# Kernel tuning notes

Hardware: AMD Instinct MI355X
Metric: run time of the kernel (lower is better)

The kernel has to match this reference:

```python
import jax, jax.numpy as jnp
import numpy as np

H = 16       # num_heads
D = 128      # head_dim
SCALE = 1.0 / np.sqrt(D).astype(np.float32)


def setup_inputs() -> dict:
    key = jax.random.key(0)
    ks = jax.random.split(key, 5)
    B, S, C = 2, 2048, 2048
    x = jax.random.normal(ks[0], (B, S, C), dtype=jnp.float32)
    # nn.Linear stores weight as [out_features, in_features]; scale ~ kaiming-ish
    s = 1.0 / np.sqrt(C)
    wq = jax.random.normal(ks[1], (C, C), dtype=jnp.float32) * s
    wk = jax.random.normal(ks[2], (C, C), dtype=jnp.float32) * s
    wv = jax.random.normal(ks[3], (C, C), dtype=jnp.float32) * s
    wo = jax.random.normal(ks[4], (C, C), dtype=jnp.float32) * s
    return {"x": x, "wq": wq, "wk": wk, "wv": wv, "wo": wo}


def reference(x, wq, wk, wv, wo):
    B, S, C = x.shape
    # projections: nn.Linear(x) = x @ W.T
    q = (x @ wq.T).reshape(B, S, H, D).transpose(0, 2, 1, 3)  # [B,H,S,D]
    k = (x @ wk.T).reshape(B, S, H, D).transpose(0, 2, 1, 3)
    v = (x @ wv.T).reshape(B, S, H, D).transpose(0, 2, 1, 3)
    scores = jnp.einsum('bhqd,bhkd->bhqk', q, k) * SCALE      # [B,H,S,S]
    attn = jax.nn.softmax(scores, axis=-1)
    out = jnp.einsum('bhqk,bhkd->bhqd', attn, v)              # [B,H,S,D]
    out = out.transpose(0, 2, 1, 3).reshape(B, S, H * D)
    return out @ wo.T
```

## Files before the change

### kernel.cpp

```cpp
#include <hip/hip_runtime.h>
#include <hip/hip_bf16.h>
#include <cstdint>
#include <cstddef>

typedef __bf16 bf16_t;
typedef __bf16 bf8_t __attribute__((ext_vector_type(8)));
typedef __bf16 bf4_t __attribute__((ext_vector_type(4)));
typedef float f4_t __attribute__((ext_vector_type(4)));
typedef float f8_t __attribute__((ext_vector_type(8)));

#define DEV static __device__ __forceinline__

DEV f4_t mfma16(bf8_t a, bf8_t b, f4_t c) {
    return __builtin_amdgcn_mfma_f32_16x16x32_bf16(a, b, c, 0, 0, 0);
}

DEV bf8_t cvt8(f8_t v) {
    bf8_t r;
#pragma unroll
    for (int i = 0; i < 8; ++i) r[i] = (bf16_t)v[i];
    return r;
}

DEV void load_lds16(const bf16_t* g, bf16_t* l) {
    __builtin_amdgcn_global_load_lds(
        (const __attribute__((address_space(1))) uint32_t*)g,
        (__attribute__((address_space(3))) uint32_t*)l,
        16, 0, 0);
}

__global__ __launch_bounds__(256) void cvt_fused(const float* __restrict__ x,
                                                 const float* __restrict__ wq,
                                                 const float* __restrict__ wk,
                                                 const float* __restrict__ wv,
                                                 bf16_t* __restrict__ xb,
                                                 bf16_t* __restrict__ wqkvb) {
    const int bid = blockIdx.x;
    const float* src;
    bf16_t* dst;
    int base;
    if (bid < 4096) {
        src = x; dst = xb; base = bid;
    } else {
        const int seg = (bid - 4096) >> 11;
        src = (seg == 0) ? wq : (seg == 1) ? wk : wv;
        dst = wqkvb + (size_t)seg * 4194304;
        base = (bid - 4096) & 2047;
    }
    const size_t i = ((size_t)base * 256 + threadIdx.x) * 8;
    const f8_t v = *(const f8_t*)&src[i];
    *(bf8_t*)&dst[i] = cvt8(v);
}

__global__ __launch_bounds__(256) void cvt_bf16(const float* __restrict__ in,
                                                bf16_t* __restrict__ out, int n8) {
    const int i = blockIdx.x * 256 + threadIdx.x;
    if (i < n8) {
        const f8_t v = *(const f8_t*)&in[(size_t)i * 8];
        *(bf8_t*)&out[(size_t)i * 8] = cvt8(v);
    }
}

DEV void stage_half(const bf16_t* X, int row0, int rb, int kt, bf16_t* bufX,
                    int wave, int srow, int scol) {
#pragma unroll
    for (int kk = 0; kk < 2; ++kk)
        load_lds16(X + (size_t)(row0 + rb + wave * 16 + srow) * 2048 + kt * 64 + kk * 32 + scol,
                   bufX + kk * 8192 + (rb + wave * 16) * 32);
}

__global__ __launch_bounds__(512, 2) void gemm_qk(const bf16_t* __restrict__ A,
                                                  const bf16_t* __restrict__ B,
                                                  bf16_t* __restrict__ Cq,
                                                  bf16_t* __restrict__ Ck) {
    __shared__ bf16_t smem[65536];

    const int tid = threadIdx.x, lane = tid & 63, wave = tid >> 6;
    const int wr = wave >> 2, wc = wave & 3;
    const int q4 = lane >> 4, r16 = lane & 15;
    const int srow = lane >> 2;
    const int scol = ((lane & 3) ^ ((lane >> 3) & 3)) * 8;
    const int rkey = (r16 >> 1) & 3;

    int wg = blockIdx.y * 16 + blockIdx.x;
    wg = (wg & 7) * 32 + (wg >> 3);
    const int bm0 = (wg / 16) * 256;
    const int bn0 = (wg % 16) * 256;

    f4_t acc[8][4] = {};

    {
        bf16_t* b0 = smem;
        bf16_t* b1 = smem + 32768;
        stage_half(A, bm0, 0,   0, b0,          wave, srow, scol);
        stage_half(A, bm0, 128, 0, b0,          wave, srow, scol);
        stage_half(B, bn0, 0,   0, b0 + 16384,  wave, srow, scol);
        stage_half(B, bn0, 128, 0, b0 + 16384,  wave, srow, scol);
        stage_half(B, bn0, 0,   1, b1 + 16384,  wave, srow, scol);
        stage_half(B, bn0, 128, 1, b1 + 16384,  wave, srow, scol);
        asm volatile("s_waitcnt vmcnt(4)" ::: "memory");
        __builtin_amdgcn_s_barrier();
    }

    for (int t = 0; t < 32; ++t) {
        bf16_t* buf  = smem + (t & 1) * 32768;
        bf16_t* bufN = smem + ((t + 1) & 1) * 32768;

        bf8_t bq[4][2];
#pragma unroll
        for (int p = 0; p < 4; ++p) {
            if (p == 0) {
#pragma unroll
                for (int n = 0; n < 4; ++n)
#pragma unroll
                    for (int kk = 0; kk < 2; ++kk)
                        bq[n][kk] = *(const bf8_t*)&buf[16384 + kk * 8192 +
                                                       (wc * 64 + n * 16 + r16) * 32 +
                                                       (q4 ^ rkey) * 8];
            }
            bf8_t af[2][2];
#pragma unroll
            for (int i = 0; i < 2; ++i)
#pragma unroll
                for (int kk = 0; kk < 2; ++kk)
                    af[i][kk] = *(const bf8_t*)&buf[kk * 8192 +
                                                    (wr * 128 + (2 * p + i) * 16 + r16) * 32 +
                                                    (q4 ^ rkey) * 8];

            if (p == 0 && t + 1 < 32) {
                stage_half(A, bm0, 0,   t + 1, bufN, wave, srow, scol);
                stage_half(A, bm0, 128, t + 1, bufN, wave, srow, scol);
            }
            if (p == 1 && t + 2 < 32)
                stage_half(B, bn0, 0,   t + 2, buf + 16384, wave, srow, scol);
            if (p == 2 && t + 2 < 32)
                stage_half(B, bn0, 128, t + 2, buf + 16384, wave, srow, scol);

            __builtin_amdgcn_s_barrier();
            asm volatile("s_waitcnt lgkmcnt(0)" ::: "memory");
            __builtin_amdgcn_s_setprio(1);
#pragma unroll
            for (int kk = 0; kk < 2; ++kk)
#pragma unroll
                for (int i = 0; i < 2; ++i)
#pragma unroll
                    for (int n = 0; n < 4; ++n)
                        acc[2 * p + i][n] = mfma16(af[i][kk], bq[n][kk], acc[2 * p + i][n]);
            __builtin_amdgcn_s_setprio(0);
            if (p == 3) {
                if (t < 30) {
                    asm volatile("s_waitcnt vmcnt(4)" ::: "memory");
                } else {
                    asm volatile("s_waitcnt vmcnt(0)" ::: "memory");
                }
            }
            __builtin_amdgcn_s_barrier();
        }
    }

    __syncthreads();

    bf16_t* strip = smem + wave * 4608;
    bf16_t* dst = (bn0 < 2048) ? Cq : Ck;
    const int nb = (bn0 & 2047) + wc * 64;
#pragma unroll
    for (int P = 0; P < 2; ++P) {
#pragma unroll
        for (int i = 0; i < 4; ++i)
#pragma unroll
            for (int n = 0; n < 4; ++n)
#pragma unroll
                for (int r = 0; r < 4; ++r)
                    strip[(i * 16 + q4 * 4 + r) * 72 + n * 16 + r16] =
                        (bf16_t)acc[P * 4 + i][n][r];
        asm volatile("s_waitcnt lgkmcnt(0)" ::: "memory");
#pragma unroll
        for (int it = 0; it < 8; ++it) {
            const int row = it * 8 + (lane >> 3);
            const int c = (lane & 7) * 8;
            *(bf8_t*)&dst[(size_t)(bm0 + wr * 128 + P * 64 + row) * 2048 + nb + c] =
                *(const bf8_t*)&strip[row * 72 + c];
        }
        asm volatile("s_waitcnt lgkmcnt(0)" ::: "memory");
    }
}

__global__ __launch_bounds__(512, 2) void gemm_v(const bf16_t* __restrict__ A,
                                                 const bf16_t* __restrict__ B,
                                                 bf16_t* __restrict__ Cv) {
    __shared__ bf16_t smem[73728];

    const int tid = threadIdx.x, lane = tid & 63, wave = tid >> 6;
    const int wr = wave >> 2, wc = wave & 3;
    const int q4 = lane >> 4, r16 = lane & 15;
    const int srow = lane >> 2;
    const int scol = ((lane & 3) ^ ((lane >> 3) & 3)) * 8;
    const int rkey = (r16 >> 1) & 3;

    int wg = blockIdx.y * 8 + blockIdx.x;
    wg = (wg & 7) * 32 + (wg >> 3);
    const int bm0 = (wg / 8) * 128;
    const int bn0 = (wg % 8) * 256;

    f4_t acc[4][4] = {};

    auto stageA = [&](int kt, bf16_t* buf) {
#pragma unroll
        for (int kk = 0; kk < 2; ++kk)
            load_lds16(A + (size_t)(bm0 + wave * 16 + srow) * 2048 + kt * 64 + kk * 32 + scol,
                       buf + kk * 4096 + wave * 16 * 32);
    };
    auto stageB = [&](int kt, bf16_t* buf, int rb) {
#pragma unroll
        for (int kk = 0; kk < 2; ++kk)
            load_lds16(B + (size_t)(bn0 + rb + wave * 16 + srow) * 2048 + kt * 64 + kk * 32 + scol,
                       buf + 8192 + kk * 8192 + (rb + wave * 16) * 32);
    };

    {
        stageA(0, smem);
        stageB(0, smem, 0);
        stageB(0, smem, 128);
        stageA(1, smem + 24576);
        stageB(1, smem + 24576, 0);
        stageB(1, smem + 24576, 128);
        asm volatile("s_waitcnt vmcnt(6)" ::: "memory");
        __builtin_amdgcn_s_barrier();
    }

    int cb = 0, sb = 2;
    for (int t = 0; t < 32; ++t) {
        bf16_t* buf  = smem + cb * 24576;
        bf16_t* sbuf = smem + sb * 24576;

        {
            bf8_t af[4], bq[4];
#pragma unroll
            for (int i = 0; i < 4; ++i)
                af[i] = *(const bf8_t*)&buf[(wr * 64 + i * 16 + r16) * 32 + (q4 ^ rkey) * 8];
#pragma unroll
            for (int n = 0; n < 4; ++n)
                bq[n] = *(const bf8_t*)&buf[8192 + (wc * 64 + n * 16 + r16) * 32 +
                                            (q4 ^ rkey) * 8];
            if (t + 2 < 32) {
                stageA(t + 2, sbuf);
                stageB(t + 2, sbuf, 0);
            }
            __builtin_amdgcn_s_barrier();
            asm volatile("s_waitcnt lgkmcnt(0)" ::: "memory");
            __builtin_amdgcn_s_setprio(1);
#pragma unroll
            for (int i = 0; i < 4; ++i)
#pragma unroll
                for (int n = 0; n < 4; ++n)
                    acc[i][n] = mfma16(af[i], bq[n], acc[i][n]);
            __builtin_amdgcn_s_setprio(0);
            __builtin_amdgcn_s_barrier();
        }

        {
            bf8_t af[4], bq[4];
#pragma unroll
            for (int i = 0; i < 4; ++i)
                af[i] = *(const bf8_t*)&buf[4096 + (wr * 64 + i * 16 + r16) * 32 +
                                            (q4 ^ rkey) * 8];
#pragma unroll
            for (int n = 0; n < 4; ++n)
                bq[n] = *(const bf8_t*)&buf[8192 + 8192 + (wc * 64 + n * 16 + r16) * 32 +
                                            (q4 ^ rkey) * 8];
            if (t + 2 < 32)
                stageB(t + 2, sbuf, 128);
            __builtin_amdgcn_s_barrier();
            asm volatile("s_waitcnt lgkmcnt(0)" ::: "memory");
            __builtin_amdgcn_s_setprio(1);
#pragma unroll
            for (int i = 0; i < 4; ++i)
#pragma unroll
                for (int n = 0; n < 4; ++n)
                    acc[i][n] = mfma16(af[i], bq[n], acc[i][n]);
            __builtin_amdgcn_s_setprio(0);
            if (t < 30) {
                asm volatile("s_waitcnt vmcnt(6)" ::: "memory");
            } else {
                asm volatile("s_waitcnt vmcnt(0)" ::: "memory");
            }
            __builtin_amdgcn_s_barrier();
        }

        cb = (cb == 2) ? 0 : cb + 1;
        sb = (sb == 2) ? 0 : sb + 1;
    }

    __syncthreads();

    bf16_t* strip = smem + wave * 4608;
    const int bb = bm0 >> 11;
    const int s0 = (bm0 & 2047) + wr * 64;
#pragma unroll
    for (int i = 0; i < 4; ++i)
#pragma unroll
        for (int n = 0; n < 4; ++n)
#pragma unroll
            for (int r = 0; r < 4; ++r)
                strip[(n * 16 + r16) * 72 + i * 16 + q4 * 4 + r] =
                    (bf16_t)acc[i][n][r];
    asm volatile("s_waitcnt lgkmcnt(0)" ::: "memory");
#pragma unroll
    for (int it = 0; it < 8; ++it) {
        const int nrow = it * 8 + (lane >> 3);
        const int c = (lane & 7) * 8;
        const int dg = bn0 + wc * 64 + nrow;
        const int h = dg >> 7, d = dg & 127;
        *(bf8_t*)&Cv[(((size_t)(bb * 16 + h) * 128 + d) << 11) + s0 + c] =
            *(const bf8_t*)&strip[nrow * 72 + c];
    }
}

__global__ __launch_bounds__(512, 2) void gemm_out(const bf16_t* __restrict__ A,
                                                   const bf16_t* __restrict__ B,
                                                   float* __restrict__ C) {
    __shared__ bf16_t smem[73728];

    const int tid = threadIdx.x, lane = tid & 63, wave = tid >> 6;
    const int wr = wave >> 2, wc = wave & 3;
    const int q4 = lane >> 4, r16 = lane & 15;
    const int srow = lane >> 2;
    const int scol = ((lane & 3) ^ ((lane >> 3) & 3)) * 8;
    const int rkey = (r16 >> 1) & 3;

    int wg = blockIdx.y * 8 + blockIdx.x;
    wg = (wg & 7) * 32 + (wg >> 3);
    const int bm0 = (wg / 8) * 128;
    const int bn0 = (wg % 8) * 256;

    f4_t acc[4][4] = {};

    auto stageA = [&](int kt, bf16_t* buf) {
#pragma unroll
        for (int kk = 0; kk < 2; ++kk)
            load_lds16(A + (size_t)(bm0 + wave * 16 + srow) * 2048 + kt * 64 + kk * 32 + scol,
                       buf + kk * 4096 + wave * 16 * 32);
    };
    auto stageB = [&](int kt, bf16_t* buf, int rb) {
#pragma unroll
        for (int kk = 0; kk < 2; ++kk)
            load_lds16(B + (size_t)(bn0 + rb + wave * 16 + srow) * 2048 + kt * 64 + kk * 32 + scol,
                       buf + 8192 + kk * 8192 + (rb + wave * 16) * 32);
    };

    {
        stageA(0, smem);
        stageB(0, smem, 0);
        stageB(0, smem, 128);
        stageA(1, smem + 24576);
        stageB(1, smem + 24576, 0);
        stageB(1, smem + 24576, 128);
        asm volatile("s_waitcnt vmcnt(6)" ::: "memory");
        __builtin_amdgcn_s_barrier();
    }

    int cb = 0, sb = 2;
    for (int t = 0; t < 32; ++t) {
        bf16_t* buf  = smem + cb * 24576;
        bf16_t* sbuf = smem + sb * 24576;

        {
            bf8_t af[4], bq[4];
#pragma unroll
            for (int i = 0; i < 4; ++i)
                af[i] = *(const bf8_t*)&buf[(wr * 64 + i * 16 + r16) * 32 + (q4 ^ rkey) * 8];
#pragma unroll
            for (int n = 0; n < 4; ++n)
                bq[n] = *(const bf8_t*)&buf[8192 + (wc * 64 + n * 16 + r16) * 32 +
                                            (q4 ^ rkey) * 8];
            if (t + 2 < 32) {
                stageA(t + 2, sbuf);
                stageB(t + 2, sbuf, 0);
            }
            __builtin_amdgcn_s_barrier();
            asm volatile("s_waitcnt lgkmcnt(0)" ::: "memory");
            __builtin_amdgcn_s_setprio(1);
#pragma unroll
            for (int i = 0; i < 4; ++i)
#pragma unroll
                for (int n = 0; n < 4; ++n)
                    acc[i][n] = mfma16(af[i], bq[n], acc[i][n]);
            __builtin_amdgcn_s_setprio(0);
            __builtin_amdgcn_s_barrier();
        }

        {
            bf8_t af[4], bq[4];
#pragma unroll
            for (int i = 0; i < 4; ++i)
                af[i] = *(const bf8_t*)&buf[4096 + (wr * 64 + i * 16 + r16) * 32 +
                                            (q4 ^ rkey) * 8];
#pragma unroll
            for (int n = 0; n < 4; ++n)
                bq[n] = *(const bf8_t*)&buf[8192 + 8192 + (wc * 64 + n * 16 + r16) * 32 +
                                            (q4 ^ rkey) * 8];
            if (t + 2 < 32)
                stageB(t + 2, sbuf, 128);
            __builtin_amdgcn_s_barrier();
            asm volatile("s_waitcnt lgkmcnt(0)" ::: "memory");
            __builtin_amdgcn_s_setprio(1);
#pragma unroll
            for (int i = 0; i < 4; ++i)
#pragma unroll
                for (int n = 0; n < 4; ++n)
                    acc[i][n] = mfma16(af[i], bq[n], acc[i][n]);
            __builtin_amdgcn_s_setprio(0);
            if (t < 30) {
                asm volatile("s_waitcnt vmcnt(6)" ::: "memory");
            } else {
                asm volatile("s_waitcnt vmcnt(0)" ::: "memory");
            }
            __builtin_amdgcn_s_barrier();
        }

        cb = (cb == 2) ? 0 : cb + 1;
        sb = (sb == 2) ? 0 : sb + 1;
    }

#pragma unroll
    for (int i = 0; i < 4; ++i)
#pragma unroll
        for (int n = 0; n < 4; ++n)
#pragma unroll
            for (int r = 0; r < 4; ++r) {
                const int m = bm0 + wr * 64 + i * 16 + q4 * 4 + r;
                const int nn = bn0 + wc * 64 + n * 16 + r16;
                C[(size_t)m * 2048 + nn] = acc[i][n][r];
            }
}

__global__ __launch_bounds__(256) void flash5(const bf16_t* __restrict__ Q,
                                              const bf16_t* __restrict__ K,
                                              const bf16_t* __restrict__ VT,
                                              bf16_t* __restrict__ O) {
    constexpr int S = 2048, C = 2048;
    constexpr float SCL = 0.08838834764831845f * 1.4426950408889634f;
    __shared__ bf16_t Ks[4 * 64 * 32];
    __shared__ bf16_t Vs[2 * 128 * 32];
    __shared__ bf16_t Ps[4][32 * 72];

    const int tid = threadIdx.x, lane = tid & 63, wave = tid >> 6;
    const int q4 = lane >> 4, r16 = lane & 15;
    const int bh = blockIdx.y, b = bh >> 4, h = bh & 15;
    const int q0 = blockIdx.x * 128 + wave * 32;

    const size_t qrow = (size_t)b * S + q0;
    const bf16_t* Qp0 = Q + (qrow + r16) * C + h * 128;
    const bf16_t* Qp1 = Q + (qrow + 16 + r16) * C + h * 128;
    const bf16_t* Kbase = K + (size_t)b * S * C + h * 128;
    const bf16_t* Vbase = VT + (size_t)bh * 128 * S;
    bf16_t* Pw = &Ps[wave][0];

    const int srow = lane >> 2;
    const int scol = (((lane & 3) ^ ((lane >> 3) & 3))) * 8;
    const int rkey = (r16 >> 1) & 3;

    bf8_t aq0[4], aq1[4];
#pragma unroll
    for (int kk = 0; kk < 4; ++kk) {
        aq0[kk] = *(const bf8_t*)&Qp0[kk * 32 + q4 * 8];
        aq1[kk] = *(const bf8_t*)&Qp1[kk * 32 + q4 * 8];
    }

    bf8_t ones;
#pragma unroll
    for (int i = 0; i < 8; ++i) ones[i] = (bf16_t)1.0f;

    f4_t o0[8] = {}, o1[8] = {};
    f4_t lacc0 = {}, lacc1 = {};

    for (int kv0 = 0; kv0 < S; kv0 += 64) {
        __syncthreads();
#pragma unroll
        for (int r0 = 0; r0 < 64; r0 += 16)
            load_lds16(Kbase + (size_t)(kv0 + r0 + srow) * C + wave * 32 + scol,
                       Ks + wave * 2048 + r0 * 32);
        {
            const int kkp = wave >> 1;
            const int rb = (wave & 1) * 64;
#pragma unroll
            for (int r0 = 0; r0 < 64; r0 += 16)
                load_lds16(Vbase + (size_t)(rb + r0 + srow) * S + kv0 + kkp * 32 + scol,
                           Vs + kkp * 4096 + (rb + r0) * 32);
        }
        __syncthreads();

        f4_t s4a[4] = {}, s4b[4] = {};
#pragma unroll
        for (int kk = 0; kk < 4; ++kk) {
#pragma unroll
            for (int j = 0; j < 4; ++j) {
                const bf8_t bk =
                    *(const bf8_t*)&Ks[kk * 2048 + (j * 16 + r16) * 32 + (q4 ^ rkey) * 8];
                s4a[j] = mfma16(bk, aq0[kk], s4a[j]);
                s4b[j] = mfma16(bk, aq1[kk], s4b[j]);
            }
        }

#pragma unroll
        for (int j = 0; j < 4; ++j) {
            bf4_t pa, pb;
#pragma unroll
            for (int r = 0; r < 4; ++r) {
                pa[r] = (bf16_t)exp2f(s4a[j][r] * SCL);
                pb[r] = (bf16_t)exp2f(s4b[j][r] * SCL);
            }
            *(bf4_t*)&Pw[r16 * 72 + j * 16 + q4 * 4] = pa;
            *(bf4_t*)&Pw[(16 + r16) * 72 + j * 16 + q4 * 4] = pb;
        }
        asm volatile("s_waitcnt lgkmcnt(0)" ::: "memory");

        bf8_t ap0[2], ap1[2];
#pragma unroll
        for (int kkp = 0; kkp < 2; ++kkp) {
            ap0[kkp] = *(const bf8_t*)&Pw[r16 * 72 + kkp * 32 + q4 * 8];
            ap1[kkp] = *(const bf8_t*)&Pw[(16 + r16) * 72 + kkp * 32 + q4 * 8];
        }

#pragma unroll
        for (int kkp = 0; kkp < 2; ++kkp) {
            lacc0 = mfma16(ap0[kkp], ones, lacc0);
            lacc1 = mfma16(ap1[kkp], ones, lacc1);
        }

#pragma unroll
        for (int t = 0; t < 8; ++t) {
#pragma unroll
            for (int kkp = 0; kkp < 2; ++kkp) {
                const bf8_t bv =
                    *(const bf8_t*)&Vs[kkp * 4096 + (t * 16 + r16) * 32 + (q4 ^ rkey) * 8];
                o0[t] = mfma16(ap0[kkp], bv, o0[t]);
                o1[t] = mfma16(ap1[kkp], bv, o1[t]);
            }
        }
    }

    f4_t inv0, inv1;
#pragma unroll
    for (int r = 0; r < 4; ++r) {
        inv0[r] = 1.0f / lacc0[r];
        inv1[r] = 1.0f / lacc1[r];
    }
#pragma unroll
    for (int t = 0; t < 8; ++t)
#pragma unroll
        for (int r = 0; r < 4; ++r) {
            O[(qrow + q4 * 4 + r) * C + h * 128 + t * 16 + r16] = (bf16_t)(o0[t][r] * inv0[r]);
            O[(qrow + 16 + q4 * 4 + r) * C + h * 128 + t * 16 + r16] =
                (bf16_t)(o1[t][r] * inv1[r]);
        }
}

extern "C" void kernel_launch(void* const* d_in, const int* in_sizes, int n_in,
                              void* d_out, int out_size, void* d_ws, size_t ws_size,
                              hipStream_t stream) {
    const float* x  = (const float*)d_in[0];
    const float* wq = (const float*)d_in[1];
    const float* wk = (const float*)d_in[2];
    const float* wv = (const float*)d_in[3];
    const float* wo = (const float*)d_in[4];

    bf16_t* ws = (bf16_t*)d_ws;
    bf16_t* xb   = ws;
    bf16_t* Wqkv = ws + 8388608;
    bf16_t* Qb   = ws + 20971520;
    bf16_t* Kb   = ws + 29360128;
    bf16_t* Vt   = ws + 37748736;
    bf16_t* Wob  = xb;
    bf16_t* At   = Wqkv;

    cvt_fused<<<10240, 256, 0, stream>>>(x, wq, wk, wv, xb, Wqkv);

    gemm_qk<<<dim3(16, 16), 512, 0, stream>>>(xb, Wqkv, Qb, Kb);

    gemm_v<<<dim3(8, 32), 512, 0, stream>>>(xb, Wqkv + 8388608, Vt);

    cvt_bf16<<<2048, 256, 0, stream>>>(wo, Wob, 524288);

    flash5<<<dim3(16, 32), 256, 0, stream>>>(Qb, Kb, Vt, At);

    gemm_out<<<dim3(8, 32), 512, 0, stream>>>(At, Wob, (float*)d_out);
}
```

Before: 363.2 us.

## Prefetch next K/V tile into registers while computing current attention tile

The attention kernel no longer loads each K/V tile into LDS at the top of the loop between two barriers. It now issues global loads for the next tile into registers before the QK^T, softmax and PV MFMAs of the current tile, then writes them to LDS after the compute. The first tile is staged before the loop. This is meant to hide global-memory latency behind matrix work, at the cost of extra VGPRs for the prefetch buffers, which could reduce occupancy.

```diff
diff --git a/kernel.cpp b/kernel.cpp
--- a/kernel.cpp
+++ b/kernel.cpp
@@ -459,6 +459,11 @@
     const int srow = lane >> 2;
     const int scol = (((lane & 3) ^ ((lane >> 3) & 3))) * 8;
     const int rkey = (r16 >> 1) & 3;
+    const int vkk = wave >> 1;
+    const int vrb = (wave & 1) * 64;
+
+    bf16_t* KsW = Ks + wave * 2048;
+    bf16_t* VsW = Vs + vkk * 4096;
 
     bf8_t aq0[4], aq1[4];
 #pragma unroll
@@ -474,21 +479,31 @@
     f4_t o0[8] = {}, o1[8] = {};
     f4_t lacc0 = {}, lacc1 = {};
 
+#pragma unroll
+    for (int r0 = 0; r0 < 64; r0 += 16)
+        load_lds16(Kbase + (size_t)(r0 + srow) * C + wave * 32 + scol, KsW + r0 * 32);
+#pragma unroll
+    for (int r0 = 0; r0 < 64; r0 += 16)
+        load_lds16(Vbase + (size_t)(vrb + r0 + srow) * S + vkk * 32 + scol,
+                   VsW + (vrb + r0) * 32);
+    __syncthreads();
+
     for (int kv0 = 0; kv0 < S; kv0 += 64) {
-        __syncthreads();
-#pragma unroll
-        for (int r0 = 0; r0 < 64; r0 += 16)
-            load_lds16(Kbase + (size_t)(kv0 + r0 + srow) * C + wave * 32 + scol,
-                       Ks + wave * 2048 + r0 * 32);
-        {
-            const int kkp = wave >> 1;
-            const int rb = (wave & 1) * 64;
-#pragma unroll
-            for (int r0 = 0; r0 < 64; r0 += 16)
-                load_lds16(Vbase + (size_t)(rb + r0 + srow) * S + kv0 + kkp * 32 + scol,
-                           Vs + kkp * 4096 + (rb + r0) * 32);
-        }
-        __syncthreads();
+        const bool more = (kv0 + 64 < S);
+
+        bf8_t kreg[4], vreg[4];
+        if (more) {
+            const int nkv = kv0 + 64;
+#pragma unroll
+            for (int i = 0; i < 4; ++i)
+                kreg[i] = *(const bf8_t*)&Kbase[(size_t)(nkv + i * 16 + srow) * C +
+                                                wave * 32 + scol];
+#pragma unroll
+            for (int i = 0; i < 4; ++i)
+                vreg[i] = *(const bf8_t*)&Vbase[(size_t)(vrb + i * 16 + srow) * S +
+                                                nkv + vkk * 32 + scol];
+            __builtin_amdgcn_sched_barrier(0);
+        }
 
         f4_t s4a[4] = {}, s4b[4] = {};
 #pragma unroll
@@ -537,6 +552,17 @@
                 o0[t] = mfma16(ap0[kkp], bv, o0[t]);
                 o1[t] = mfma16(ap1[kkp], bv, o1[t]);
             }
+        }
+
+        if (more) {
+            __syncthreads();
+#pragma unroll
+            for (int i = 0; i < 4; ++i)
+                *(bf8_t*)&KsW[i * 16 * 32 + lane * 8] = kreg[i];
+#pragma unroll
+            for (int i = 0; i < 4; ++i)
+                *(bf8_t*)&VsW[(vrb + i * 16) * 32 + lane * 8] = vreg[i];
+            __syncthreads();
         }
     }
 
```

Measured after the change: 405.8 us. 11.7% more time.
